# Kernel optimization log

Hardware: AMD Instinct MI355X
Metric: run time of the kernel (lower is better)

The kernel has to match this reference:

```python
import jax, jax.numpy as jnp
import numpy as np

B_LARGE, B_SMALL = 256, 256
R_LARGE, R_SMALL = 64, 16
N_LARGE, N_SMALL = 128, 128
D = 4096


def setup_inputs() -> dict:
    key = jax.random.key(0)
    k1, k2, k3, k4, k5 = jax.random.split(key, 5)
    x = jax.random.normal(k1, (B_LARGE + B_SMALL, 1, D), dtype=jnp.float16)
    wids_large = jax.random.randint(k2, (B_LARGE,), 0, N_LARGE, dtype=jnp.int32)
    wids_small = jax.random.randint(k3, (B_SMALL,), 0, N_SMALL, dtype=jnp.int32)
    lora_A_large = (jax.random.normal(k4, (N_LARGE, D, R_LARGE), dtype=jnp.float16) * jnp.float16(0.02))
    lora_A_small = (jax.random.normal(k5, (N_SMALL, D, R_SMALL), dtype=jnp.float16) * jnp.float16(0.02))
    return {"x": x, "wids_large": wids_large, "wids_small": wids_small,
            "lora_A_large": lora_A_large, "lora_A_small": lora_A_small}


def reference(x, wids_large, wids_small, lora_A_large, lora_A_small):
    # split batch into large / small adapter groups
    x_l = x[:B_LARGE]          # [Bl, 1, D]
    x_s = x[B_LARGE:]          # [Bs, 1, D]
    # gather per-sample adapter matrices, then batched matmul (BGMV pattern)
    A_l = lora_A_large[wids_large]   # [Bl, D, r_large]
    A_s = lora_A_small[wids_small]   # [Bs, D, r_small]
    y_large = jnp.einsum('bsd,bdr->bsr', x_l, A_l)  # [Bl, 1, r_large]
    y_small = jnp.einsum('bsd,bdr->bsr', x_s, A_s)  # [Bs, 1, r_small]
    return (y_large, y_small)
```

## Files before the change

### kernel.cpp

```cpp
#include <hip/hip_runtime.h>

#define NDIM 4096
#define B_LG 256
#define B_SM 256
#define N_WID 128
#define R_LG 64
#define R_SM 16
#define BLOCK 1024
#define MAXB 256
#define TD 2048
#define MG 4

#define WS_CNT_L 0
#define WS_CNT_S 128
#define WS_BKT_L 256
#define WS_BKT_S (256 + N_WID * MAXB)

__global__ __launch_bounds__(256)
void bucket_kernel(const int* __restrict__ wids_l,
                   const int* __restrict__ wids_s,
                   int* __restrict__ ws)
{
    __shared__ int cl[N_WID], cs[N_WID];
    const int t = threadIdx.x;
    if (t < N_WID) { cl[t] = 0; cs[t] = 0; }
    __syncthreads();
    {
        const int w = wids_l[t];
        const int slot = atomicAdd(&cl[w], 1);
        ws[WS_BKT_L + w * MAXB + slot] = t;
    }
    {
        const int w = wids_s[t];
        const int slot = atomicAdd(&cs[w], 1);
        ws[WS_BKT_S + w * MAXB + slot] = t;
    }
    __syncthreads();
    if (t < N_WID) { ws[WS_CNT_L + t] = cl[t]; ws[WS_CNT_S + t] = cs[t]; }
}

template<int R, int M>
__device__ __forceinline__ void gemv_group(
    const float* __restrict__ x,
    const float* __restrict__ Ab,
    float* __restrict__ outb,
    const int* __restrict__ batches,
    float* __restrict__ xs,
    float* __restrict__ red,
    int* __restrict__ row_lds)
{
    constexpr int LPR  = R / 4;
    constexpr int ROWS = BLOCK / LPR;
    constexpr int IT   = TD / ROWS;

    const int t = threadIdx.x;
    int rows[M];
#pragma unroll
    for (int m = 0; m < M; ++m) rows[m] = batches[m];
    if (t < M) row_lds[t] = rows[t];

    const int d_sub  = t / LPR;
    const int r_base = (t % LPR) * 4;

    float acc[M][4];
#pragma unroll
    for (int m = 0; m < M; ++m)
#pragma unroll
        for (int j = 0; j < 4; ++j) acc[m][j] = 0.0f;

    for (int dt = 0; dt < NDIM; dt += TD) {
        __syncthreads();
        for (int i = t; i < M * (TD / 4); i += BLOCK) {
            const int m   = i >> 9;
            const int idx = i & 511;
            reinterpret_cast<float4*>(xs + m * TD)[idx] =
                reinterpret_cast<const float4*>(x + (size_t)row_lds[m] * NDIM + dt)[idx];
        }
        __syncthreads();

        const float* Abt = Ab + (size_t)dt * R;
#pragma unroll 4
        for (int i = 0; i < IT; ++i) {
            const int d = i * ROWS + d_sub;
            const float4 av = *reinterpret_cast<const float4*>(Abt + (size_t)d * R + r_base);
#pragma unroll
            for (int m = 0; m < M; ++m) {
                const float xv = xs[m * TD + d];
                acc[m][0] = fmaf(xv, av.x, acc[m][0]);
                acc[m][1] = fmaf(xv, av.y, acc[m][1]);
                acc[m][2] = fmaf(xv, av.z, acc[m][2]);
                acc[m][3] = fmaf(xv, av.w, acc[m][3]);
            }
        }
    }

    const int wave = t >> 6;
    const int lane = t & 63;
#pragma unroll
    for (int m = 0; m < M; ++m)
#pragma unroll
        for (int off = 32; off >= LPR; off >>= 1)
#pragma unroll
            for (int j = 0; j < 4; ++j)
                acc[m][j] += __shfl_down(acc[m][j], off, 64);

#pragma unroll
    for (int m = 0; m < M; ++m) {
        __syncthreads();
        if (lane < LPR)
#pragma unroll
            for (int j = 0; j < 4; ++j) red[(wave * 16 + lane) * 4 + j] = acc[m][j];
        __syncthreads();
        if (t < R) {
            const int rl = t / 4, j = t % 4;
            float v = 0.0f;
#pragma unroll
            for (int w = 0; w < 16; ++w) v += red[(w * 16 + rl) * 4 + j];
            outb[(size_t)rows[m] * R + t] = v;
        }
    }
}

template<int R>
__device__ __forceinline__ void run_wid(
    const float* x, const float* Ab, float* outb,
    const int* bucket, int count, int half,
    float* xs, float* red, int* row_lds)
{
    for (int g = half * MG; g < count; g += 2 * MG) {
        const int M = min(MG, count - g);
        const int* b = bucket + g;
        switch (M) {
            case 1: gemv_group<R, 1>(x, Ab, outb, b, xs, red, row_lds); break;
            case 2: gemv_group<R, 2>(x, Ab, outb, b, xs, red, row_lds); break;
            case 3: gemv_group<R, 3>(x, Ab, outb, b, xs, red, row_lds); break;
            default: gemv_group<R, 4>(x, Ab, outb, b, xs, red, row_lds); break;
        }
    }
}

__global__ __launch_bounds__(BLOCK, 8)
void SequentialLoraA_kernel(const float* __restrict__ x,
                            const float* __restrict__ Al,
                            const float* __restrict__ As,
                            float* __restrict__ out,
                            const int* __restrict__ ws)
{
    __shared__ float xs[MG * TD];
    __shared__ float red[16 * 16 * 4];
    __shared__ int row_lds[MG];

    const int blk  = blockIdx.x;
    const int half = blk & 1;

    if (blk < 2 * N_WID) {
        const int wid = blk >> 1;
        const int count = ws[WS_CNT_L + wid];
        run_wid<R_LG>(x,
                      Al + (size_t)wid * NDIM * R_LG,
                      out,
                      ws + WS_BKT_L + wid * MAXB, count, half,
                      xs, red, row_lds);
    } else {
        const int wid = (blk - 2 * N_WID) >> 1;
        const int count = ws[WS_CNT_S + wid];
        run_wid<R_SM>(x + (size_t)B_LG * NDIM,
                      As + (size_t)wid * NDIM * R_SM,
                      out + (size_t)B_LG * R_LG,
                      ws + WS_BKT_S + wid * MAXB, count, half,
                      xs, red, row_lds);
    }
}

extern "C" void kernel_launch(void* const* d_in, const int* in_sizes, int n_in,
                              void* d_out, int out_size, void* d_ws, size_t ws_size,
                              hipStream_t stream) {
    const float* x      = (const float*)d_in[0];
    const int*   wids_l = (const int*)d_in[1];
    const int*   wids_s = (const int*)d_in[2];
    const float* Al     = (const float*)d_in[3];
    const float* As     = (const float*)d_in[4];
    float* out = (float*)d_out;
    int*   ws  = (int*)d_ws;

    bucket_kernel<<<1, 256, 0, stream>>>(wids_l, wids_s, ws);
    SequentialLoraA_kernel<<<4 * N_WID, BLOCK, 0, stream>>>(x, Al, As, out, ws);
}
```

Measured before the change: 234.0 us.

## Split each adapter's work along D halves with atomic accumulation and register prefetch

Each adapter was handled by two blocks that split its batch rows into alternating groups, each block reading the full D range of A. Now each block takes one half of D and processes every row for that adapter, so each block streams only half of the A matrix. Partial sums are combined with atomicAdd into an output that the setup kernel zeroes first. The inner loop also prefetches several A float4 loads into registers before the FMAs. This adds atomics and a zeroing pass, and the lower launch-bounds occupancy hint may change register allocation.

```diff
diff --git a/kernel.cpp b/kernel.cpp
--- a/kernel.cpp
+++ b/kernel.cpp
@@ -1,6 +1,7 @@
 #include <hip/hip_runtime.h>
 
 #define NDIM 4096
+#define HALF 2048
 #define B_LG 256
 #define B_SM 256
 #define N_WID 128
@@ -8,59 +9,73 @@
 #define R_SM 16
 #define BLOCK 1024
 #define MAXB 256
-#define TD 2048
 #define MG 4
+#define PF 4
+#define OUT_SIZE (B_LG * R_LG + B_SM * R_SM)
 
 #define WS_CNT_L 0
 #define WS_CNT_S 128
 #define WS_BKT_L 256
 #define WS_BKT_S (256 + N_WID * MAXB)
 
-__global__ __launch_bounds__(256)
-void bucket_kernel(const int* __restrict__ wids_l,
-                   const int* __restrict__ wids_s,
-                   int* __restrict__ ws)
+__global__ __launch_bounds__(BLOCK)
+void setup_kernel(const int* __restrict__ wids_l,
+                  const int* __restrict__ wids_s,
+                  int* __restrict__ ws,
+                  float* __restrict__ out)
 {
     __shared__ int cl[N_WID], cs[N_WID];
     const int t = threadIdx.x;
     if (t < N_WID) { cl[t] = 0; cs[t] = 0; }
     __syncthreads();
-    {
+    if (t < B_LG) {
         const int w = wids_l[t];
-        const int slot = atomicAdd(&cl[w], 1);
-        ws[WS_BKT_L + w * MAXB + slot] = t;
-    }
-    {
-        const int w = wids_s[t];
-        const int slot = atomicAdd(&cs[w], 1);
-        ws[WS_BKT_S + w * MAXB + slot] = t;
+        const int s = atomicAdd(&cl[w], 1);
+        ws[WS_BKT_L + w * MAXB + s] = t;
+    } else if (t < B_LG + B_SM) {
+        const int b = t - B_LG;
+        const int w = wids_s[b];
+        const int s = atomicAdd(&cs[w], 1);
+        ws[WS_BKT_S + w * MAXB + s] = b;
     }
     __syncthreads();
     if (t < N_WID) { ws[WS_CNT_L + t] = cl[t]; ws[WS_CNT_S + t] = cs[t]; }
+    for (int i = t; i < OUT_SIZE; i += BLOCK) out[i] = 0.0f;
 }
 
 template<int R, int M>
-__device__ __forceinline__ void gemv_group(
+__device__ __forceinline__ void gemv_half(
     const float* __restrict__ x,
     const float* __restrict__ Ab,
     float* __restrict__ outb,
     const int* __restrict__ batches,
+    int d0,
     float* __restrict__ xs,
-    float* __restrict__ red,
-    int* __restrict__ row_lds)
+    float* __restrict__ red)
 {
     constexpr int LPR  = R / 4;
     constexpr int ROWS = BLOCK / LPR;
-    constexpr int IT   = TD / ROWS;
+    constexpr int IT   = HALF / ROWS;
 
     const int t = threadIdx.x;
+
     int rows[M];
 #pragma unroll
     for (int m = 0; m < M; ++m) rows[m] = batches[m];
-    if (t < M) row_lds[t] = rows[t];
+
+    __syncthreads();
+#pragma unroll
+    for (int m = 0; m < M; ++m) {
+        if (t < HALF / 4) {
+            reinterpret_cast<float4*>(xs + m * HALF)[t] =
+                reinterpret_cast<const float4*>(x + (size_t)rows[m] * NDIM + d0)[t];
+        }
+    }
+    __syncthreads();
 
     const int d_sub  = t / LPR;
     const int r_base = (t % LPR) * 4;
+    const float* Abt = Ab + (size_t)d0 * R + r_base;
 
     float acc[M][4];
 #pragma unroll
@@ -68,28 +83,23 @@
 #pragma unroll
         for (int j = 0; j < 4; ++j) acc[m][j] = 0.0f;
 
-    for (int dt = 0; dt < NDIM; dt += TD) {
-        __syncthreads();
-        for (int i = t; i < M * (TD / 4); i += BLOCK) {
-            const int m   = i >> 9;
-            const int idx = i & 511;
-            reinterpret_cast<float4*>(xs + m * TD)[idx] =
-                reinterpret_cast<const float4*>(x + (size_t)row_lds[m] * NDIM + dt)[idx];
+    for (int ig = 0; ig < IT; ig += PF) {
+        float4 pf[PF];
+#pragma unroll
+        for (int p = 0; p < PF; ++p) {
+            const int d = (ig + p) * ROWS + d_sub;
+            pf[p] = *reinterpret_cast<const float4*>(Abt + (size_t)d * R);
         }
-        __syncthreads();
-
-        const float* Abt = Ab + (size_t)dt * R;
-#pragma unroll 4
-        for (int i = 0; i < IT; ++i) {
-            const int d = i * ROWS + d_sub;
-            const float4 av = *reinterpret_cast<const float4*>(Abt + (size_t)d * R + r_base);
+#pragma unroll
+        for (int p = 0; p < PF; ++p) {
+            const int d = (ig + p) * ROWS + d_sub;
 #pragma unroll
             for (int m = 0; m < M; ++m) {
-                const float xv = xs[m * TD + d];
-                acc[m][0] = fmaf(xv, av.x, acc[m][0]);
-                acc[m][1] = fmaf(xv, av.y, acc[m][1]);
-                acc[m][2] = fmaf(xv, av.z, acc[m][2]);
-                acc[m][3] = fmaf(xv, av.w, acc[m][3]);
+                const float xv = xs[m * HALF + d];
+                acc[m][0] = fmaf(xv, pf[p].x, acc[m][0]);
+                acc[m][1] = fmaf(xv, pf[p].y, acc[m][1]);
+                acc[m][2] = fmaf(xv, pf[p].z, acc[m][2]);
+                acc[m][3] = fmaf(xv, pf[p].w, acc[m][3]);
             }
         }
     }
@@ -116,59 +126,58 @@
             float v = 0.0f;
 #pragma unroll
             for (int w = 0; w < 16; ++w) v += red[(w * 16 + rl) * 4 + j];
-            outb[(size_t)rows[m] * R + t] = v;
+            atomicAdd(outb + (size_t)rows[m] * R + t, v);
         }
     }
 }
 
 template<int R>
-__device__ __forceinline__ void run_wid(
+__device__ __forceinline__ void run_wid_half(
     const float* x, const float* Ab, float* outb,
-    const int* bucket, int count, int half,
-    float* xs, float* red, int* row_lds)
+    const int* bucket, int count, int d0,
+    float* xs, float* red)
 {
-    for (int g = half * MG; g < count; g += 2 * MG) {
+    for (int g = 0; g < count; g += MG) {
         const int M = min(MG, count - g);
         const int* b = bucket + g;
         switch (M) {
-            case 1: gemv_group<R, 1>(x, Ab, outb, b, xs, red, row_lds); break;
-            case 2: gemv_group<R, 2>(x, Ab, outb, b, xs, red, row_lds); break;
-            case 3: gemv_group<R, 3>(x, Ab, outb, b, xs, red, row_lds); break;
-            default: gemv_group<R, 4>(x, Ab, outb, b, xs, red, row_lds); break;
+            case 1: gemv_half<R, 1>(x, Ab, outb, b, d0, xs, red); break;
+            case 2: gemv_half<R, 2>(x, Ab, outb, b, d0, xs, red); break;
+            case 3: gemv_half<R, 3>(x, Ab, outb, b, d0, xs, red); break;
+            default: gemv_half<R, 4>(x, Ab, outb, b, d0, xs, red); break;
         }
     }
 }
 
-__global__ __launch_bounds__(BLOCK, 8)
+__global__ __launch_bounds__(BLOCK, 4)
 void SequentialLoraA_kernel(const float* __restrict__ x,
                             const float* __restrict__ Al,
                             const float* __restrict__ As,
                             float* __restrict__ out,
                             const int* __restrict__ ws)
 {
-    __shared__ float xs[MG * TD];
+    __shared__ float xs[MG * HALF];
     __shared__ float red[16 * 16 * 4];
-    __shared__ int row_lds[MG];
 
     const int blk  = blockIdx.x;
-    const int half = blk & 1;
-
     if (blk < 2 * N_WID) {
-        const int wid = blk >> 1;
+        const int wid  = blk >> 1;
+        const int d0   = (blk & 1) * HALF;
         const int count = ws[WS_CNT_L + wid];
-        run_wid<R_LG>(x,
-                      Al + (size_t)wid * NDIM * R_LG,
-                      out,
-                      ws + WS_BKT_L + wid * MAXB, count, half,
-                      xs, red, row_lds);
+        run_wid_half<R_LG>(x,
+                           Al + (size_t)wid * NDIM * R_LG,
+                           out,
+                           ws + WS_BKT_L + wid * MAXB, count, d0,
+                           xs, red);
     } else {
-        const int wid = (blk - 2 * N_WID) >> 1;
+        const int wid  = (blk - 2 * N_WID) >> 1;
+        const int d0   = (blk & 1) * HALF;
         const int count = ws[WS_CNT_S + wid];
-        run_wid<R_SM>(x + (size_t)B_LG * NDIM,
-                      As + (size_t)wid * NDIM * R_SM,
-                      out + (size_t)B_LG * R_LG,
-                      ws + WS_BKT_S + wid * MAXB, count, half,
-                      xs, red, row_lds);
+        run_wid_half<R_SM>(x + (size_t)B_LG * NDIM,
+                           As + (size_t)wid * NDIM * R_SM,
+                           out + (size_t)B_LG * R_LG,
+                           ws + WS_BKT_S + wid * MAXB, count, d0,
+                           xs, red);
     }
 }
 
@@ -183,6 +192,6 @@
     float* out = (float*)d_out;
     int*   ws  = (int*)d_ws;
 
-    bucket_kernel<<<1, 256, 0, stream>>>(wids_l, wids_s, ws);
+    setup_kernel<<<1, BLOCK, 0, stream>>>(wids_l, wids_s, ws, out);
     SequentialLoraA_kernel<<<4 * N_WID, BLOCK, 0, stream>>>(x, Al, As, out, ws);
 }
```

Result: faster. 228.9 us (-2.2%).
